# Kernel optimization log

Hardware: AMD Instinct MI355X
Metric: run time of the kernel (lower is better)

The kernel has to match this reference:

```python
import jax, jax.numpy as jnp
import numpy as np

N = 100000        # nnode
F = 128           # in_features
E = 1600000       # num edges (avg degree 16)
HOP = 3
ALPHA = 0.1       # alpha_ (float -> takes the non-None branch)
LEAKY = 0.2


def setup_inputs() -> dict:
    key = jax.random.key(0)
    k1, k2, k3, k4, k5, k6, k7 = jax.random.split(key, 7)
    x = jax.random.normal(k1, (N, F), dtype=jnp.float32)
    h0 = jax.random.normal(k2, (N, F), dtype=jnp.float32)
    a = jax.random.normal(k3, (2 * F, 1), dtype=jnp.float32) * (1.414 / np.sqrt(2 * F))
    temp = jnp.zeros((HOP + 1,), dtype=jnp.float32)
    # cheb init: alp*(1-alp)^k with alp=0.9, last entry (1-alp)^2
    alp = 0.9
    cheb = np.array([alp * (1 - alp) ** k for k in range(HOP + 1)], dtype=np.float32)
    cheb[-1] = (1 - alp) ** 2
    cheb = jnp.asarray(cheb)
    adj_vals = jax.random.uniform(k4, (E,), dtype=jnp.float32)
    edge_row = jax.random.randint(k5, (E,), 0, N, dtype=jnp.int32)
    edge_col = jax.random.randint(k6, (E,), 0, N, dtype=jnp.int32)
    return {"x": x, "h0": h0, "a": a, "temp": temp, "cheb": cheb,
            "adj_vals": adj_vals, "edge_row": edge_row, "edge_col": edge_col}


def _edge_softmax(e, row, n):
    # row-wise (dim=1) sparse softmax over edge values
    m = jax.ops.segment_max(e, row, num_segments=n)
    ex = jnp.exp(e - m[row])
    s = jax.ops.segment_sum(ex, row, num_segments=n)
    return ex / s[row]


def reference(x, h0, a, temp, cheb, adj_vals, edge_row, edge_col):
    n, f = x.shape
    # --- attention: e[i,j] = leakyrelu((x @ a1)[i] + (x @ a2)[j]) on edges only ---
    feat_1 = (x @ a[:f]).squeeze(-1)   # [N]
    feat_2 = (x @ a[f:]).squeeze(-1)   # [N]
    e = feat_1[edge_row] + feat_2[edge_col]          # [E]
    e = jnp.where(e >= 0, e, LEAKY * e)               # leaky_relu(0.2)
    U_vals = _edge_softmax(e, edge_row, n)            # sparse softmax over rows
    P_vals = 0.5 * U_vals

    # --- lifting bases ---
    cheb_coe = jax.nn.sigmoid(cheb)
    # rowsum of (adj \u2299 P)
    rowsum = jax.ops.segment_sum(adj_vals * P_vals, edge_row, num_segments=n)  # [N]

    update = x
    feat_prime = x
    for step in range(HOP):
        # sparse mm: update <- U @ update
        update = jax.ops.segment_sum(U_vals[:, None] * update[edge_col],
                                     edge_row, num_segments=n)  # [N,F]
        feat_even_bar = update                       # alpha_ is not None branch
        if step >= 1:
            rowsum = cheb_coe[step - 1] * rowsum
        feat_odd_bar = update - feat_even_bar * rowsum[:, None]
        feat_fuse = ALPHA * feat_even_bar + (1.0 - ALPHA) * feat_odd_bar
        if step == 0:
            feat_prime = ALPHA * x + (1.0 - ALPHA) * feat_fuse
        else:
            feat_prime = ALPHA * feat_prime + (1.0 - ALPHA) * feat_fuse
    return feat_prime
```

## Files before the change

### kernel.cpp

```cpp
#include <hip/hip_runtime.h>
#include <hip/hip_fp16.h>

#define F 128
#define ALPHA 0.1f
#define BETA  0.9f
#define LEAKY 0.2f

#define RSH 8
#define RB  256
#define BT  4096
#define CAP 6400
#define CMASK 0x1FFFF

__global__ __launch_bounds__(256) void zero_ints(int* __restrict__ p, int n) {
    int i = blockIdx.x * 256 + threadIdx.x;
    int st = gridDim.x * 256;
    for (; i < n; i += st) p[i] = 0;
}

__global__ __launch_bounds__(256) void featconv(const float* __restrict__ x,
                                                const float* __restrict__ a,
                                                float* __restrict__ f1,
                                                float* __restrict__ f2,
                                                __half2* __restrict__ xh, int n) {
    int w = (blockIdx.x * blockDim.x + threadIdx.x) >> 6;
    int lane = threadIdx.x & 63;
    if (w >= n) return;
    const float2* xr = (const float2*)(x + (size_t)w * F);
    float2 v  = xr[lane];
    float2 A1 = ((const float2*)a)[lane];
    float2 A2 = ((const float2*)a)[64 + lane];
    float d1 = v.x * A1.x + v.y * A1.y;
    float d2 = v.x * A2.x + v.y * A2.y;
    for (int o = 32; o; o >>= 1) {
        d1 += __shfl_xor(d1, o);
        d2 += __shfl_xor(d2, o);
    }
    xh[(size_t)w * 64 + lane] = __float22half2_rn(v);
    if (lane == 0) { f1[w] = d1; f2[w] = d2; }
}

__global__ __launch_bounds__(256) void bucket_hist(const int* __restrict__ erow,
                                                   int* __restrict__ bcnt, int e, int nb) {
    __shared__ int h[512];
    h[threadIdx.x] = 0; h[256 + threadIdx.x] = 0;
    __syncthreads();
    int i = blockIdx.x * 256 + threadIdx.x;
    int st = gridDim.x * 256;
    for (; i < e; i += st) atomicAdd(&h[erow[i] >> RSH], 1);
    __syncthreads();
    for (int b = threadIdx.x; b < nb; b += 256)
        if (h[b]) atomicAdd(&bcnt[b], h[b]);
}

__global__ __launch_bounds__(256) void bucket_scan(const int* __restrict__ bcnt,
                                                   int* __restrict__ base,
                                                   int* __restrict__ cursor,
                                                   int* __restrict__ rowptr_n,
                                                   int nb, int e) {
    __shared__ int arr[256];
    int t = threadIdx.x;
    int v0 = (2 * t     < nb) ? bcnt[2 * t]     : 0;
    int v1 = (2 * t + 1 < nb) ? bcnt[2 * t + 1] : 0;
    int ps = v0 + v1;
    arr[t] = ps; __syncthreads();
    for (int off = 1; off < 256; off <<= 1) {
        int add = (t >= off) ? arr[t - off] : 0;
        __syncthreads();
        arr[t] += add;
        __syncthreads();
    }
    int ex = arr[t] - ps;
    if (2 * t     <= nb) { base[2 * t]     = ex;      cursor[2 * t]     = ex; }
    if (2 * t + 1 <= nb) { base[2 * t + 1] = ex + v0; cursor[2 * t + 1] = ex + v0; }
    if (t == 255) *rowptr_n = e;
}

__global__ __launch_bounds__(256) void bin_edges(const int* __restrict__ erow,
                                                 const int* __restrict__ ecol,
                                                 const float* __restrict__ adj,
                                                 int* __restrict__ cursor,
                                                 int2* __restrict__ binned, int e) {
    __shared__ int tcnt[512], toff[512], res[512], tcur[512];
    __shared__ int arr[256];
    __shared__ short sidx[BT];
    int tid = threadIdx.x;
    int i0 = blockIdx.x * BT;
    int m = e - i0; if (m > BT) m = BT;
    tcnt[tid] = 0; tcnt[256 + tid] = 0;
    __syncthreads();
    for (int k = tid; k < m; k += 256) atomicAdd(&tcnt[erow[i0 + k] >> RSH], 1);
    __syncthreads();
    int v0 = tcnt[2 * tid], v1 = tcnt[2 * tid + 1];
    int ps = v0 + v1;
    arr[tid] = ps; __syncthreads();
    for (int off = 1; off < 256; off <<= 1) {
        int add = (tid >= off) ? arr[tid - off] : 0;
        __syncthreads();
        arr[tid] += add;
        __syncthreads();
    }
    int ex = arr[tid] - ps;
    toff[2 * tid] = ex; toff[2 * tid + 1] = ex + v0;
    __syncthreads();
    for (int b = tid; b < 512; b += 256) {
        if (tcnt[b] > 0) res[b] = atomicAdd(&cursor[b], tcnt[b]);
        tcur[b] = 0;
    }
    __syncthreads();
    for (int k = tid; k < m; k += 256) {
        int b = erow[i0 + k] >> RSH;
        int rk = atomicAdd(&tcur[b], 1);
        sidx[toff[b] + rk] = (short)k;
    }
    __syncthreads();
    for (int j = tid; j < m; j += 256) {
        int k = sidx[j];
        int i = i0 + k;
        int r = erow[i];
        int b = r >> RSH;
        int dst = res[b] + (j - toff[b]);
        binned[dst] = make_int2(((r & (RB - 1)) << 17) | ecol[i], __float_as_int(adj[i]));
    }
}

__global__ __launch_bounds__(256) void build_csr(const int2* __restrict__ binned,
                                                 const int* __restrict__ bbase,
                                                 const float* __restrict__ f1,
                                                 const float* __restrict__ f2,
                                                 int2* __restrict__ csr,
                                                 int* __restrict__ rowptr,
                                                 float* __restrict__ sden,
                                                 float* __restrict__ rsg, int n) {
    int k = blockIdx.x;
    int row0 = k << RSH;
    int nr = n - row0; if (nr > RB) nr = RB;
    int m0 = bbase[k];
    int m = bbase[k + 1] - m0; if (m > CAP) m = CAP;
    int tid = threadIdx.x;
    __shared__ int   cnt[RB], cur[RB], rpl[RB], arr[256];
    __shared__ float f1l[RB], sl[RB], rsl[RB];
    __shared__ int2  seg[CAP];
    cnt[tid] = 0; cur[tid] = 0; sl[tid] = 0.f; rsl[tid] = 0.f;
    f1l[tid] = (tid < nr) ? f1[row0 + tid] : 0.f;
    __syncthreads();
    for (int t = tid; t < m; t += 256) atomicAdd(&cnt[(binned[m0 + t].x >> 17) & 0xFF], 1);
    __syncthreads();
    int v = cnt[tid];
    arr[tid] = v; __syncthreads();
    for (int off = 1; off < 256; off <<= 1) {
        int add = (tid >= off) ? arr[tid - off] : 0;
        __syncthreads();
        arr[tid] += add;
        __syncthreads();
    }
    rpl[tid] = arr[tid] - v;
    __syncthreads();
    if (tid < nr) rowptr[row0 + tid] = m0 + rpl[tid];
    for (int t = tid; t < m; t += 256) {
        int2 w = binned[m0 + t];
        int rl = (w.x >> 17) & 0xFF;
        int c  = w.x & CMASK;
        float tt = f1l[rl] + f2[c];
        tt = (tt >= 0.f) ? tt : LEAKY * tt;
        float exv = __expf(tt);
        int pos = atomicAdd(&cur[rl], 1);
        seg[rpl[rl] + pos] = make_int2(c, __float_as_int(exv));
        atomicAdd(&sl[rl], exv);
        atomicAdd(&rsl[rl], 0.5f * __int_as_float(w.y) * exv);
    }
    __syncthreads();
    for (int t = tid; t < m; t += 256) csr[m0 + t] = seg[t];
    if (tid < nr) { sden[row0 + tid] = sl[tid]; rsg[row0 + tid] = rsl[tid]; }
}

__global__ __launch_bounds__(256) void spmm_fuse(const __half2* __restrict__ upd_in,
                                                 __half2* __restrict__ upd_out,
                                                 const __half2* __restrict__ xh,
                                                 const __half2* __restrict__ g1h,
                                                 float* __restrict__ out,
                                                 const int2* __restrict__ csr,
                                                 const int* __restrict__ rowptr,
                                                 const float* __restrict__ sden,
                                                 const float* __restrict__ rs,
                                                 const float* __restrict__ cheb,
                                                 int n, int final_hop) {
    int r = blockIdx.x * 4 + (threadIdx.x >> 6);
    int lane = threadIdx.x & 63;
    if (r >= n) return;
    int sp = rowptr[r];
    int deg = rowptr[r + 1] - sp;

    float2 acc = make_float2(0.f, 0.f);
    for (int base = 0; base < deg; base += 64) {
        int mm = deg - base; if (mm > 64) mm = 64;
        int2 ed = (lane < mm) ? csr[sp + base + lane] : make_int2(0, 0);
        int mm8 = (mm + 7) & ~7;
        for (int j = 0; j < mm8; j += 8) {
            float2 g[8]; float u[8];
            #pragma unroll
            for (int kk = 0; kk < 8; kk++) {
                int c  = __shfl(ed.x, j + kk) & CMASK;
                u[kk]  = __int_as_float(__shfl(ed.y, j + kk));
                g[kk]  = __half22float2(upd_in[(size_t)c * 64 + lane]);
            }
            #pragma unroll
            for (int kk = 0; kk < 8; kk++) {
                acc.x += u[kk] * g[kk].x;
                acc.y += u[kk] * g[kk].y;
            }
        }
    }

    float sr = sden[r];
    float inv = (sr > 0.f) ? 1.f / sr : 0.f;
    float gx = acc.x * inv, gy = acc.y * inv;
    size_t idx = (size_t)r * 64 + lane;

    if (!final_hop) {
        upd_out[idx] = __float22half2_rn(make_float2(gx, gy));
    } else {
        float rsum = rs[r] * inv;
        float s0 = 1.f / (1.f + __expf(-cheb[0]));
        float s1 = 1.f / (1.f + __expf(-cheb[1]));
        float c0 = 1.f - BETA * rsum;
        float c1 = 1.f - BETA * rsum * s0;
        float c2 = 1.f - BETA * rsum * s0 * s1;
        float2 xv = __half22float2(xh[idx]);
        float2 g1 = __half22float2(g1h[idx]);
        float2 g2 = __half22float2(upd_in[idx]);
        float2 o;
        o.x = 0.001f * xv.x + 0.009f * c0 * g1.x + 0.09f * c1 * g2.x + 0.9f * c2 * gx;
        o.y = 0.001f * xv.y + 0.009f * c0 * g1.y + 0.09f * c1 * g2.y + 0.9f * c2 * gy;
        ((float2*)out)[idx] = o;
    }
}

extern "C" void kernel_launch(void* const* d_in, const int* in_sizes, int n_in,
                              void* d_out, int out_size, void* d_ws, size_t ws_size,
                              hipStream_t stream) {
    const float* x    = (const float*)d_in[0];
    const float* a    = (const float*)d_in[2];
    const float* cheb = (const float*)d_in[4];
    const float* adj  = (const float*)d_in[5];
    const int*   erow = (const int*)d_in[6];
    const int*   ecol = (const int*)d_in[7];
    int n = in_sizes[0] / F;
    int e = in_sizes[5];
    float* out = (float*)d_out;
    int nb = (n + RB - 1) >> RSH;

    float* ws = (float*)d_ws;
    size_t NH = (size_t)n * 64;
    int2*    csr  = (int2*)ws;
    __half2* xh   = (__half2*)(ws + 2 * (size_t)e);
    __half2* u1h  = xh + NH;
    __half2* u2h  = u1h + NH;
    int2*    binned = (int2*)u2h;
    float* f1     = (float*)(u2h + NH);
    float* f2     = f1 + n;
    float* sden   = f2 + n;
    float* rs     = sden + n;
    int*   rowptr = (int*)(rs + n);
    int*   bcnt   = rowptr + n + 1;
    int*   bbase  = bcnt + 512;
    int*   bcur   = bbase + 513;

    int wave_blocks = (n + 3) / 4;

    hipLaunchKernelGGL(zero_ints, dim3(4), dim3(256), 0, stream, bcnt, nb);
    hipLaunchKernelGGL(featconv, dim3(wave_blocks), dim3(256), 0, stream, x, a, f1, f2, xh, n);
    hipLaunchKernelGGL(bucket_hist, dim3(1024), dim3(256), 0, stream, erow, bcnt, e, nb);
    hipLaunchKernelGGL(bucket_scan, dim3(1), dim3(256), 0, stream, bcnt, bbase, bcur, rowptr + n, nb, e);
    hipLaunchKernelGGL(bin_edges, dim3((e + BT - 1) / BT), dim3(256), 0, stream,
                       erow, ecol, adj, bcur, binned, e);
    hipLaunchKernelGGL(build_csr, dim3(nb), dim3(256), 0, stream,
                       binned, bbase, f1, f2, csr, rowptr, sden, rs, n);

    hipLaunchKernelGGL(spmm_fuse, dim3(wave_blocks), dim3(256), 0, stream,
                       xh, u1h, (const __half2*)nullptr, (const __half2*)nullptr,
                       (float*)nullptr, csr, rowptr, sden, rs, cheb, n, 0);
    hipLaunchKernelGGL(spmm_fuse, dim3(wave_blocks), dim3(256), 0, stream,
                       u1h, u2h, (const __half2*)nullptr, (const __half2*)nullptr,
                       (float*)nullptr, csr, rowptr, sden, rs, cheb, n, 0);
    hipLaunchKernelGGL(spmm_fuse, dim3(wave_blocks), dim3(256), 0, stream,
                       u2h, (__half2*)nullptr, xh, u1h,
                       out, csr, rowptr, sden, rs, cheb, n, 1);
}
```

Baseline: 310.6 us.

## Shrink CSR buckets to 64 rows and scatter directly to global CSR

Reduces rows per bucket from 256 to 64, raising the bucket count to about 1563, and resizes the histogram, scan and binning arrays to match. build_csr no longer stages the row segment in a large shared-memory buffer and writes CSR entries straight to global memory, which drops the CAP truncation and the shared-memory occupancy limit. The aim is more parallelism and occupancy in CSR construction. The cost is more global atomics on the bucket cursors in bin_edges, scattered global writes, and an extra async memcpy to set the final rowptr entry.

```diff
diff --git a/kernel.cpp b/kernel.cpp
--- a/kernel.cpp
+++ b/kernel.cpp
@@ -2,14 +2,13 @@
 #include <hip/hip_fp16.h>
 
 #define F 128
-#define ALPHA 0.1f
 #define BETA  0.9f
 #define LEAKY 0.2f
 
-#define RSH 8
-#define RB  256
-#define BT  4096
-#define CAP 6400
+#define BSH 6
+#define RPB 64
+#define NBMAX 2048
+#define BT  2048
 #define CMASK 0x1FFFF
 
 __global__ __launch_bounds__(256) void zero_ints(int* __restrict__ p, int n) {
@@ -42,29 +41,28 @@
 
 __global__ __launch_bounds__(256) void bucket_hist(const int* __restrict__ erow,
                                                    int* __restrict__ bcnt, int e, int nb) {
-    __shared__ int h[512];
-    h[threadIdx.x] = 0; h[256 + threadIdx.x] = 0;
+    __shared__ int h[NBMAX];
+    for (int b = threadIdx.x; b < NBMAX; b += 256) h[b] = 0;
     __syncthreads();
     int i = blockIdx.x * 256 + threadIdx.x;
     int st = gridDim.x * 256;
-    for (; i < e; i += st) atomicAdd(&h[erow[i] >> RSH], 1);
+    for (; i < e; i += st) atomicAdd(&h[erow[i] >> BSH], 1);
     __syncthreads();
     for (int b = threadIdx.x; b < nb; b += 256)
         if (h[b]) atomicAdd(&bcnt[b], h[b]);
 }
 
-__global__ __launch_bounds__(256) void bucket_scan(const int* __restrict__ bcnt,
-                                                   int* __restrict__ base,
-                                                   int* __restrict__ cursor,
-                                                   int* __restrict__ rowptr_n,
-                                                   int nb, int e) {
-    __shared__ int arr[256];
+__global__ __launch_bounds__(1024) void bucket_scan(const int* __restrict__ bcnt,
+                                                    int* __restrict__ base,
+                                                    int* __restrict__ cursor,
+                                                    int nb) {
+    __shared__ int arr[1024];
     int t = threadIdx.x;
     int v0 = (2 * t     < nb) ? bcnt[2 * t]     : 0;
     int v1 = (2 * t + 1 < nb) ? bcnt[2 * t + 1] : 0;
     int ps = v0 + v1;
     arr[t] = ps; __syncthreads();
-    for (int off = 1; off < 256; off <<= 1) {
+    for (int off = 1; off < 1024; off <<= 1) {
         int add = (t >= off) ? arr[t - off] : 0;
         __syncthreads();
         arr[t] += add;
@@ -73,7 +71,6 @@
     int ex = arr[t] - ps;
     if (2 * t     <= nb) { base[2 * t]     = ex;      cursor[2 * t]     = ex; }
     if (2 * t + 1 <= nb) { base[2 * t + 1] = ex + v0; cursor[2 * t + 1] = ex + v0; }
-    if (t == 255) *rowptr_n = e;
 }
 
 __global__ __launch_bounds__(256) void bin_edges(const int* __restrict__ erow,
@@ -81,35 +78,37 @@
                                                  const float* __restrict__ adj,
                                                  int* __restrict__ cursor,
                                                  int2* __restrict__ binned, int e) {
-    __shared__ int tcnt[512], toff[512], res[512], tcur[512];
+    __shared__ int tcnt[NBMAX], toff[NBMAX], res[NBMAX], tcur[NBMAX];
     __shared__ int arr[256];
     __shared__ short sidx[BT];
     int tid = threadIdx.x;
     int i0 = blockIdx.x * BT;
     int m = e - i0; if (m > BT) m = BT;
-    tcnt[tid] = 0; tcnt[256 + tid] = 0;
-    __syncthreads();
-    for (int k = tid; k < m; k += 256) atomicAdd(&tcnt[erow[i0 + k] >> RSH], 1);
-    __syncthreads();
-    int v0 = tcnt[2 * tid], v1 = tcnt[2 * tid + 1];
-    int ps = v0 + v1;
-    arr[tid] = ps; __syncthreads();
+    for (int b = tid; b < NBMAX; b += 256) tcnt[b] = 0;
+    __syncthreads();
+    for (int k = tid; k < m; k += 256) atomicAdd(&tcnt[erow[i0 + k] >> BSH], 1);
+    __syncthreads();
+    int loc[8]; int s8 = 0; int b8 = tid * 8;
+    #pragma unroll
+    for (int k = 0; k < 8; k++) { loc[k] = tcnt[b8 + k]; s8 += loc[k]; }
+    arr[tid] = s8; __syncthreads();
     for (int off = 1; off < 256; off <<= 1) {
         int add = (tid >= off) ? arr[tid - off] : 0;
         __syncthreads();
         arr[tid] += add;
         __syncthreads();
     }
-    int ex = arr[tid] - ps;
-    toff[2 * tid] = ex; toff[2 * tid + 1] = ex + v0;
-    __syncthreads();
-    for (int b = tid; b < 512; b += 256) {
+    int ex = arr[tid] - s8;
+    #pragma unroll
+    for (int k = 0; k < 8; k++) { toff[b8 + k] = ex; ex += loc[k]; }
+    __syncthreads();
+    for (int b = tid; b < NBMAX; b += 256) {
         if (tcnt[b] > 0) res[b] = atomicAdd(&cursor[b], tcnt[b]);
         tcur[b] = 0;
     }
     __syncthreads();
     for (int k = tid; k < m; k += 256) {
-        int b = erow[i0 + k] >> RSH;
+        int b = erow[i0 + k] >> BSH;
         int rk = atomicAdd(&tcur[b], 1);
         sidx[toff[b] + rk] = (short)k;
     }
@@ -118,9 +117,9 @@
         int k = sidx[j];
         int i = i0 + k;
         int r = erow[i];
-        int b = r >> RSH;
+        int b = r >> BSH;
         int dst = res[b] + (j - toff[b]);
-        binned[dst] = make_int2(((r & (RB - 1)) << 17) | ecol[i], __float_as_int(adj[i]));
+        binned[dst] = make_int2(((r & (RPB - 1)) << 17) | ecol[i], __float_as_int(adj[i]));
     }
 }
 
@@ -133,44 +132,45 @@
                                                  float* __restrict__ sden,
                                                  float* __restrict__ rsg, int n) {
     int k = blockIdx.x;
-    int row0 = k << RSH;
-    int nr = n - row0; if (nr > RB) nr = RB;
+    int row0 = k << BSH;
+    int nr = n - row0; if (nr > RPB) nr = RPB;
     int m0 = bbase[k];
-    int m = bbase[k + 1] - m0; if (m > CAP) m = CAP;
+    int m = bbase[k + 1] - m0;
     int tid = threadIdx.x;
-    __shared__ int   cnt[RB], cur[RB], rpl[RB], arr[256];
-    __shared__ float f1l[RB], sl[RB], rsl[RB];
-    __shared__ int2  seg[CAP];
-    cnt[tid] = 0; cur[tid] = 0; sl[tid] = 0.f; rsl[tid] = 0.f;
-    f1l[tid] = (tid < nr) ? f1[row0 + tid] : 0.f;
-    __syncthreads();
-    for (int t = tid; t < m; t += 256) atomicAdd(&cnt[(binned[m0 + t].x >> 17) & 0xFF], 1);
-    __syncthreads();
-    int v = cnt[tid];
-    arr[tid] = v; __syncthreads();
-    for (int off = 1; off < 256; off <<= 1) {
-        int add = (tid >= off) ? arr[tid - off] : 0;
-        __syncthreads();
-        arr[tid] += add;
-        __syncthreads();
-    }
-    rpl[tid] = arr[tid] - v;
+    __shared__ int   cnt[RPB], cur[RPB], rpl[RPB];
+    __shared__ float f1l[RPB], sl[RPB], rsl[RPB];
+    if (tid < RPB) {
+        cnt[tid] = 0; cur[tid] = 0; sl[tid] = 0.f; rsl[tid] = 0.f;
+        f1l[tid] = (tid < nr) ? f1[row0 + tid] : 0.f;
+    }
+    __syncthreads();
+    for (int t = tid; t < m; t += 256) atomicAdd(&cnt[(binned[m0 + t].x >> 17) & (RPB - 1)], 1);
+    __syncthreads();
+    if (tid < RPB) rpl[tid] = cnt[tid];
+    __syncthreads();
+    for (int off = 1; off < RPB; off <<= 1) {
+        int add = 0;
+        if (tid < RPB && tid >= off) add = rpl[tid - off];
+        __syncthreads();
+        if (tid < RPB) rpl[tid] += add;
+        __syncthreads();
+    }
+    if (tid < RPB) rpl[tid] -= cnt[tid];
     __syncthreads();
     if (tid < nr) rowptr[row0 + tid] = m0 + rpl[tid];
     for (int t = tid; t < m; t += 256) {
         int2 w = binned[m0 + t];
-        int rl = (w.x >> 17) & 0xFF;
+        int rl = (w.x >> 17) & (RPB - 1);
         int c  = w.x & CMASK;
         float tt = f1l[rl] + f2[c];
         tt = (tt >= 0.f) ? tt : LEAKY * tt;
         float exv = __expf(tt);
         int pos = atomicAdd(&cur[rl], 1);
-        seg[rpl[rl] + pos] = make_int2(c, __float_as_int(exv));
+        csr[m0 + rpl[rl] + pos] = make_int2(c, __float_as_int(exv));
         atomicAdd(&sl[rl], exv);
         atomicAdd(&rsl[rl], 0.5f * __int_as_float(w.y) * exv);
     }
     __syncthreads();
-    for (int t = tid; t < m; t += 256) csr[m0 + t] = seg[t];
     if (tid < nr) { sden[row0 + tid] = sl[tid]; rsg[row0 + tid] = rsl[tid]; }
 }
 
@@ -248,7 +248,7 @@
     int n = in_sizes[0] / F;
     int e = in_sizes[5];
     float* out = (float*)d_out;
-    int nb = (n + RB - 1) >> RSH;
+    int nb = (n + RPB - 1) >> BSH;
 
     float* ws = (float*)d_ws;
     size_t NH = (size_t)n * 64;
@@ -263,19 +263,20 @@
     float* rs     = sden + n;
     int*   rowptr = (int*)(rs + n);
     int*   bcnt   = rowptr + n + 1;
-    int*   bbase  = bcnt + 512;
-    int*   bcur   = bbase + 513;
+    int*   bbase  = bcnt + NBMAX;
+    int*   bcur   = bbase + NBMAX + 1;
 
     int wave_blocks = (n + 3) / 4;
 
-    hipLaunchKernelGGL(zero_ints, dim3(4), dim3(256), 0, stream, bcnt, nb);
+    hipLaunchKernelGGL(zero_ints, dim3(8), dim3(256), 0, stream, bcnt, nb);
     hipLaunchKernelGGL(featconv, dim3(wave_blocks), dim3(256), 0, stream, x, a, f1, f2, xh, n);
     hipLaunchKernelGGL(bucket_hist, dim3(1024), dim3(256), 0, stream, erow, bcnt, e, nb);
-    hipLaunchKernelGGL(bucket_scan, dim3(1), dim3(256), 0, stream, bcnt, bbase, bcur, rowptr + n, nb, e);
+    hipLaunchKernelGGL(bucket_scan, dim3(1), dim3(1024), 0, stream, bcnt, bbase, bcur, nb);
     hipLaunchKernelGGL(bin_edges, dim3((e + BT - 1) / BT), dim3(256), 0, stream,
                        erow, ecol, adj, bcur, binned, e);
     hipLaunchKernelGGL(build_csr, dim3(nb), dim3(256), 0, stream,
                        binned, bbase, f1, f2, csr, rowptr, sden, rs, n);
+    hipMemcpyAsync(rowptr + n, bbase + nb, sizeof(int), hipMemcpyDeviceToDevice, stream);
 
     hipLaunchKernelGGL(spmm_fuse, dim3(wave_blocks), dim3(256), 0, stream,
                        xh, u1h, (const __half2*)nullptr, (const __half2*)nullptr,
```

After: 340.7 us. 9.7% more time.
